# Optimization experiments

Hardware: AMD Instinct MI355X
Metric: run time of the kernel (lower is better)

The kernel has to match this reference:

```python
import jax, jax.numpy as jnp
import numpy as np

D_MODEL = 1024
NUM_HEADS = 16
D_K = D_MODEL // NUM_HEADS


def setup_inputs() -> dict:
    key = jax.random.key(0)
    ks = jax.random.split(key, 11)
    B, S, D = 2, 2048, D_MODEL
    s = 1.0 / np.sqrt(D)  # torch Linear default init scale
    inp = {
        'query': jax.random.normal(ks[0], (B, S, D), jnp.float32),
        'key': jax.random.normal(ks[1], (B, S, D), jnp.float32),
        'value': jax.random.normal(ks[2], (B, S, D), jnp.float32),
        'Wq': jax.random.uniform(ks[3], (D, D), jnp.float32, -s, s),
        'bq': jax.random.uniform(ks[4], (D,), jnp.float32, -s, s),
        'Wk': jax.random.uniform(ks[5], (D, D), jnp.float32, -s, s),
        'bk': jax.random.uniform(ks[6], (D,), jnp.float32, -s, s),
        'Wv': jax.random.uniform(ks[7], (D, D), jnp.float32, -s, s),
        'bv': jax.random.uniform(ks[8], (D,), jnp.float32, -s, s),
        'Wo': jax.random.uniform(ks[9], (D, D), jnp.float32, -s, s),
        'bo': jax.random.uniform(ks[10], (D,), jnp.float32, -s, s),
    }
    return inp


def reference(query, key, value, Wq, bq, Wk, bk, Wv, bv, Wo, bo):
    B, S, D = query.shape
    H, dk = NUM_HEADS, D_K
    # Linear projections (torch Linear: x @ W.T + b), split into heads -> [B,H,S,dk]
    Q = (query @ Wq.T + bq).reshape(B, S, H, dk).transpose(0, 2, 1, 3)
    K = (key @ Wk.T + bk).reshape(B, S, H, dk).transpose(0, 2, 1, 3)
    V = (value @ Wv.T + bv).reshape(B, S, H, dk).transpose(0, 2, 1, 3)
    scale = jnp.sqrt(jnp.asarray(dk, query.dtype))
    scores = jnp.einsum('bhqd,bhkd->bhqk', Q, K) / scale  # [B,H,S,S]
    attn = jax.nn.softmax(scores, axis=-1)
    ctx = jnp.einsum('bhqk,bhkd->bhqd', attn, V)  # [B,H,S,dk]
    ctx = ctx.transpose(0, 2, 1, 3).reshape(B, S, D)
    return ctx @ Wo.T + bo
```

## Files before the change

### kernel.cpp

```cpp
#include <hip/hip_runtime.h>

#define SEQ 2048
#define DM  1024
#define NH  16
#define DK  64
#define BATCH 2
#define MROWS (BATCH * SEQ)
#define PPITCH 72

typedef __attribute__((ext_vector_type(8))) short bf16x8;
typedef __attribute__((ext_vector_type(4))) float f32x4;

__device__ __forceinline__ float bf2f(unsigned short u) {
    union { unsigned int i; float f; } v;
    v.i = ((unsigned int)u) << 16;
    return v.f;
}

__device__ __forceinline__ unsigned short f2bf(float f) {
    union { float f; unsigned int i; } v;
    v.f = f;
    unsigned int r = v.i + 0x7FFFu + ((v.i >> 16) & 1u);
    return (unsigned short)(r >> 16);
}

__device__ __forceinline__ uint4 pack8(float4 x, float4 y) {
    uint4 r;
    r.x = (unsigned)f2bf(x.x) | ((unsigned)f2bf(x.y) << 16);
    r.y = (unsigned)f2bf(x.z) | ((unsigned)f2bf(x.w) << 16);
    r.z = (unsigned)f2bf(y.x) | ((unsigned)f2bf(y.y) << 16);
    r.w = (unsigned)f2bf(y.z) | ((unsigned)f2bf(y.w) << 16);
    return r;
}

__device__ __forceinline__ void gll16(const void* g, void* l) {
    __builtin_amdgcn_global_load_lds(
        (const __attribute__((address_space(1))) unsigned int*)g,
        (__attribute__((address_space(3))) unsigned int*)l, 16, 0, 0);
}

__global__ void detect_dtype(const unsigned short* __restrict__ q,
                             unsigned int* __restrict__ flag) {
    const int lane = threadIdx.x;
    unsigned short u = q[lane * 2];
    int e = (u >> 7) & 0xFF;
    int hit = (e >= 100 && e <= 135) ? 1 : 0;
    unsigned long long m = __ballot(hit);
    if (lane == 0) *flag = (__popcll(m) >= 48) ? 0u : 1u;
}

#define CVT_TOTAL 16781312u
struct CvtArgs {
    const void* src[11];
    unsigned short* dst[11];
};

__global__ __launch_bounds__(256) void convert_all(CvtArgs a,
                                                   const unsigned int* __restrict__ flagp) {
    const unsigned int f = *flagp;
    const size_t e0 = ((size_t)blockIdx.x * 256 + threadIdx.x) * 8;
    if (e0 >= CVT_TOTAL) return;
    const unsigned int cum[12] = {0u, 4194304u, 8388608u, 12582912u, 13631488u,
                                  14680064u, 15728640u, 16777216u, 16778240u,
                                  16779264u, 16780288u, 16781312u};
    int r = 0;
    #pragma unroll
    for (int i = 1; i < 11; ++i) r += (e0 >= cum[i]) ? 1 : 0;
    const size_t local = e0 - cum[r];
    const float sc = (r == 3 || r == 7) ? 0.125f : 1.0f;
    if (f) {
        const float* s = (const float*)a.src[r] + local;
        float4 x = *(const float4*)s;
        float4 y = *(const float4*)(s + 4);
        x.x *= sc; x.y *= sc; x.z *= sc; x.w *= sc;
        y.x *= sc; y.y *= sc; y.z *= sc; y.w *= sc;
        *(uint4*)(a.dst[r] + local) = pack8(x, y);
    } else {
        const unsigned short* s = (const unsigned short*)a.src[r] + local;
        if (sc != 1.0f) {
            unsigned short o[8];
            #pragma unroll
            for (int i = 0; i < 8; ++i) o[i] = f2bf(bf2f(s[i]) * sc);
            *(uint4*)(a.dst[r] + local) = *(const uint4*)o;
        } else {
            *(uint4*)(a.dst[r] + local) = *(const uint4*)s;
        }
    }
}

__device__ __forceinline__ void gemm_core(
    const unsigned short* __restrict__ A, const unsigned short* __restrict__ W,
    const unsigned short* __restrict__ bias, void* __restrict__ C, int cMode)
{
    __shared__ unsigned short Al[64 * 64];
    __shared__ unsigned short Bl[128 * 64];

    const int tid  = threadIdx.x;
    const int w    = tid >> 6;
    const int lane = tid & 63;
    const int lo   = lane & 15;
    const int quad = lane >> 4;
    const int bm   = blockIdx.y * 64;
    const int bn   = blockIdx.x * 128;

    const int r8  = lane >> 3;
    const int csw = ((lane ^ r8) & 7) * 8;
    const unsigned short* gA = A + (size_t)(bm + w * 16 + r8) * DM + csw;
    const unsigned short* gB = W + (size_t)(bn + w * 32 + r8) * DM + csw;
    unsigned short* lA = &Al[(w * 16) * 64];
    unsigned short* lB = &Bl[(w * 32) * 64];

    f32x4 acc[4][2];
    #pragma unroll
    for (int i = 0; i < 4; ++i)
        #pragma unroll
        for (int n = 0; n < 2; ++n) acc[i][n] = (f32x4){0.f, 0.f, 0.f, 0.f};

    const int swz = (lo & 7);

    for (int k0 = 0; k0 < DM; k0 += 64) {
        __syncthreads();
        #pragma unroll
        for (int j = 0; j < 2; ++j)
            gll16(gA + (size_t)j * 8 * DM + k0, lA + j * 8 * 64);
        #pragma unroll
        for (int j = 0; j < 4; ++j)
            gll16(gB + (size_t)j * 8 * DM + k0, lB + j * 8 * 64);
        __syncthreads();

        #pragma unroll
        for (int kc = 0; kc < 2; ++kc) {
            bf16x8 af[4], bfr[2];
            #pragma unroll
            for (int i = 0; i < 4; ++i)
                af[i] = *(const bf16x8*)&Al[(i * 16 + lo) * 64 +
                                            (((kc * 4 + quad) ^ swz) * 8)];
            #pragma unroll
            for (int n = 0; n < 2; ++n)
                bfr[n] = *(const bf16x8*)&Bl[(w * 32 + n * 16 + lo) * 64 +
                                             (((kc * 4 + quad) ^ swz) * 8)];
            #pragma unroll
            for (int i = 0; i < 4; ++i)
                #pragma unroll
                for (int n = 0; n < 2; ++n)
                    acc[i][n] = __builtin_amdgcn_mfma_f32_16x16x32_bf16(af[i], bfr[n], acc[i][n], 0, 0, 0);
        }
    }

    float bj[2];
    #pragma unroll
    for (int n = 0; n < 2; ++n)
        bj[n] = bf2f(bias[bn + w * 32 + n * 16 + lo]);

    if (cMode == 2) {
        #pragma unroll
        for (int i = 0; i < 4; ++i)
            #pragma unroll
            for (int n = 0; n < 2; ++n) {
                const int row0 = bm + i * 16 + quad * 4;
                const int col  = bn + w * 32 + n * 16 + lo;
                ushort4 cv;
                cv.x = f2bf(acc[i][n][0] + bj[n]);
                cv.y = f2bf(acc[i][n][1] + bj[n]);
                cv.z = f2bf(acc[i][n][2] + bj[n]);
                cv.w = f2bf(acc[i][n][3] + bj[n]);
                const size_t off = ((size_t)((row0 >> 11) * 16 + (col >> 6)) * 64
                                    + (col & 63)) * 2048 + (row0 & 2047);
                *(ushort4*)((unsigned short*)C + off) = cv;
            }
    } else {
        #pragma unroll
        for (int i = 0; i < 4; ++i)
            #pragma unroll
            for (int n = 0; n < 2; ++n)
                #pragma unroll
                for (int r = 0; r < 4; ++r) {
                    const int row = bm + i * 16 + quad * 4 + r;
                    const size_t off = (size_t)row * DM + bn + w * 32 + n * 16 + lo;
                    const float vv = acc[i][n][r] + bj[n];
                    if (cMode == 1) ((float*)C)[off] = vv;
                    else            ((unsigned short*)C)[off] = f2bf(vv);
                }
    }
}

__global__ __launch_bounds__(256, 4) void gemm_qkv(
    const unsigned short* __restrict__ qa, const unsigned short* __restrict__ ka,
    const unsigned short* __restrict__ va,
    const unsigned short* __restrict__ wq, const unsigned short* __restrict__ wk,
    const unsigned short* __restrict__ wv,
    const unsigned short* __restrict__ bq, const unsigned short* __restrict__ bk,
    const unsigned short* __restrict__ bv,
    unsigned short* __restrict__ oq, unsigned short* __restrict__ ok,
    unsigned short* __restrict__ ovT)
{
    if (blockIdx.z == 0)      gemm_core(qa, wq, bq, oq, 0);
    else if (blockIdx.z == 1) gemm_core(ka, wk, bk, ok, 0);
    else                      gemm_core(va, wv, bv, ovT, 2);
}

__global__ __launch_bounds__(256, 4) void gemm_out(
    const unsigned short* __restrict__ A, const unsigned short* __restrict__ W,
    const unsigned short* __restrict__ B, void* __restrict__ C,
    const unsigned int* __restrict__ flagp)
{
    gemm_core(A, W, B, C, (int)*flagp);
}

__global__ __launch_bounds__(256) void attn_mfma2(
    const unsigned short* __restrict__ Q,
    const unsigned short* __restrict__ K,
    const unsigned short* __restrict__ VT,
    unsigned short* __restrict__ CTX)
{
    __shared__ unsigned short Kl[64 * 64];
    __shared__ unsigned short Vl[64 * 64];
    __shared__ unsigned short Pl[4][2][16 * PPITCH];

    const int tid  = threadIdx.x;
    const int w    = tid >> 6;
    const int lane = tid & 63;
    const int lo   = lane & 15;
    const int quad = lane >> 4;
    const int bh = blockIdx.y;
    const int b  = bh >> 4;
    const int h  = bh & 15;
    const int q0 = blockIdx.x * 128 + w * 32;

    bf16x8 aq[2][2];
    #pragma unroll
    for (int f = 0; f < 2; ++f)
        #pragma unroll
        for (int c = 0; c < 2; ++c)
            aq[f][c] = *(const bf16x8*)(Q + (size_t)(b * SEQ + q0 + f * 16 + lo) * DM
                                        + h * 64 + c * 32 + quad * 8);

    f32x4 o[2][4];
    #pragma unroll
    for (int f = 0; f < 2; ++f)
        #pragma unroll
        for (int dt = 0; dt < 4; ++dt) o[f][dt] = (f32x4){0.f, 0.f, 0.f, 0.f};
    float lsum[2] = {0.f, 0.f};

    const int r8  = lane >> 3;
    const int csw = ((lane ^ r8) & 7) * 8;
    const int swz = lo & 7;
    const unsigned short* Kg = K + (size_t)b * SEQ * DM + h * 64;
    const unsigned short* Vg = VT + (size_t)bh * 64 * 2048;

    for (int j0 = 0; j0 < SEQ; j0 += 64) {
        __syncthreads();
        #pragma unroll
        for (int j = 0; j < 2; ++j) {
            gll16(Kg + (size_t)(j0 + w * 16 + j * 8 + r8) * DM + csw,
                  &Kl[(w * 16 + j * 8) * 64]);
            gll16(Vg + (size_t)(w * 16 + j * 8 + r8) * 2048 + j0 + csw,
                  &Vl[(w * 16 + j * 8) * 64]);
        }
        __syncthreads();

        f32x4 st[4][2];
        #pragma unroll
        for (int kt = 0; kt < 4; ++kt) {
            bf16x8 ak0 = *(const bf16x8*)&Kl[(kt * 16 + lo) * 64 + ((quad ^ swz) * 8)];
            bf16x8 ak1 = *(const bf16x8*)&Kl[(kt * 16 + lo) * 64 + (((4 + quad) ^ swz) * 8)];
            #pragma unroll
            for (int f = 0; f < 2; ++f) {
                f32x4 c = (f32x4){0.f, 0.f, 0.f, 0.f};
                c = __builtin_amdgcn_mfma_f32_16x16x32_bf16(ak0, aq[f][0], c, 0, 0, 0);
                c = __builtin_amdgcn_mfma_f32_16x16x32_bf16(ak1, aq[f][1], c, 0, 0, 0);
                st[kt][f] = c;
            }
        }

        #pragma unroll
        for (int f = 0; f < 2; ++f)
            #pragma unroll
            for (int kt = 0; kt < 4; ++kt) {
                float p0 = __expf(st[kt][f][0]), p1 = __expf(st[kt][f][1]);
                float p2 = __expf(st[kt][f][2]), p3 = __expf(st[kt][f][3]);
                lsum[f] += (p0 + p1) + (p2 + p3);
                ushort4 pv;
                pv.x = f2bf(p0); pv.y = f2bf(p1); pv.z = f2bf(p2); pv.w = f2bf(p3);
                *(ushort4*)&Pl[w][f][lo * PPITCH + kt * 16 + quad * 4] = pv;
            }
        bf16x8 ap[2][2];
        #pragma unroll
        for (int f = 0; f < 2; ++f)
            #pragma unroll
            for (int c = 0; c < 2; ++c)
                ap[f][c] = *(const bf16x8*)&Pl[w][f][lo * PPITCH + c * 32 + quad * 8];

        #pragma unroll
        for (int dt = 0; dt < 4; ++dt) {
            bf16x8 bv0 = *(const bf16x8*)&Vl[(dt * 16 + lo) * 64 + ((quad ^ swz) * 8)];
            bf16x8 bv1 = *(const bf16x8*)&Vl[(dt * 16 + lo) * 64 + (((4 + quad) ^ swz) * 8)];
            #pragma unroll
            for (int f = 0; f < 2; ++f) {
                o[f][dt] = __builtin_amdgcn_mfma_f32_16x16x32_bf16(ap[f][0], bv0, o[f][dt], 0, 0, 0);
                o[f][dt] = __builtin_amdgcn_mfma_f32_16x16x32_bf16(ap[f][1], bv1, o[f][dt], 0, 0, 0);
            }
        }
    }

    #pragma unroll
    for (int f = 0; f < 2; ++f) {
        lsum[f] += __shfl_xor(lsum[f], 16);
        lsum[f] += __shfl_xor(lsum[f], 32);
    }
    #pragma unroll
    for (int f = 0; f < 2; ++f)
        #pragma unroll
        for (int r = 0; r < 4; ++r) {
            const float lq  = __shfl(lsum[f], quad * 4 + r);
            const float inv = 1.0f / lq;
            const size_t base = (size_t)(b * SEQ + q0 + f * 16 + quad * 4 + r) * DM
                                + h * 64 + lo;
            #pragma unroll
            for (int dt = 0; dt < 4; ++dt)
                CTX[base + dt * 16] = f2bf(o[f][dt][r] * inv);
        }
}

extern "C" void kernel_launch(void* const* d_in, const int* in_sizes, int n_in,
                              void* d_out, int out_size, void* d_ws, size_t ws_size,
                              hipStream_t stream) {
    const size_t E4 = 4194304, E1 = 1048576;
    unsigned short* qb  = (unsigned short*)d_ws;
    unsigned short* kb  = qb  + E4;
    unsigned short* vb  = kb  + E4;
    unsigned short* wqb = vb  + E4;
    unsigned short* wkb = wqb + E1;
    unsigned short* wvb = wkb + E1;
    unsigned short* wob = wvb + E1;
    unsigned short* bqb = wob + E1;
    unsigned short* bkb = bqb + 1024;
    unsigned short* bvb = bkb + 1024;
    unsigned short* bob = bvb + 1024;
    unsigned short* wsQ = bob + 1024;
    unsigned short* wsK = wsQ + E4;
    unsigned short* wsVt = wsK + E4;
    unsigned int*  flag = (unsigned int*)(wsVt + E4);
    unsigned short* wsC = qb;

    detect_dtype<<<1, 64, 0, stream>>>((const unsigned short*)d_in[0], flag);

    CvtArgs ca;
    ca.src[0] = d_in[0];  ca.dst[0] = qb;
    ca.src[1] = d_in[1];  ca.dst[1] = kb;
    ca.src[2] = d_in[2];  ca.dst[2] = vb;
    ca.src[3] = d_in[3];  ca.dst[3] = wqb;
    ca.src[4] = d_in[5];  ca.dst[4] = wkb;
    ca.src[5] = d_in[7];  ca.dst[5] = wvb;
    ca.src[6] = d_in[9];  ca.dst[6] = wob;
    ca.src[7] = d_in[4];  ca.dst[7] = bqb;
    ca.src[8] = d_in[6];  ca.dst[8] = bkb;
    ca.src[9] = d_in[8];  ca.dst[9] = bvb;
    ca.src[10] = d_in[10]; ca.dst[10] = bob;
    convert_all<<<(CVT_TOTAL / 8 + 255) / 256, 256, 0, stream>>>(ca, flag);

    dim3 gq(DM / 128, MROWS / 64, 3);
    gemm_qkv<<<gq, 256, 0, stream>>>(qb, kb, vb, wqb, wkb, wvb,
                                     bqb, bkb, bvb, wsQ, wsK, wsVt);

    dim3 ga(SEQ / 128, BATCH * NH);
    attn_mfma2<<<ga, 256, 0, stream>>>(wsQ, wsK, wsVt, wsC);

    dim3 go(DM / 128, MROWS / 64);
    gemm_out<<<go, 256, 0, stream>>>(wsC, wob, bob, d_out, flag);
}
```

Before: 244.0 us.

## Use exp2 with folded log2e scale, truncating bf16 pack, and MFMA row sums

Folds log2(e)/sqrt(dk) into the Q weight/bias conversion scale so the softmax can use the native exp2 instruction directly. It replaces round-to-nearest bf16 packing of probabilities with a single byte-permute truncation. It computes the softmax denominator by multiplying the bf16 P tile against a ones vector on the matrix cores, which removes the per-element scalar adds and end-of-loop shuffles. The denominator now sums the same rounded bf16 values used in P·V, which keeps normalization consistent, but truncation adds a small bias and each tile costs extra MFMAs.

```diff
diff --git a/kernel.cpp b/kernel.cpp
--- a/kernel.cpp
+++ b/kernel.cpp
@@ -11,6 +11,8 @@
 typedef __attribute__((ext_vector_type(8))) short bf16x8;
 typedef __attribute__((ext_vector_type(4))) float f32x4;
 
+extern "C" __device__ float __ocml_native_exp2_f32(float);
+
 __device__ __forceinline__ float bf2f(unsigned short u) {
     union { unsigned int i; float f; } v;
     v.i = ((unsigned int)u) << 16;
@@ -22,6 +24,11 @@
     v.f = f;
     unsigned int r = v.i + 0x7FFFu + ((v.i >> 16) & 1u);
     return (unsigned short)(r >> 16);
+}
+
+__device__ __forceinline__ unsigned int pk_trunc(float a, float b) {
+    return __builtin_amdgcn_perm(__float_as_uint(b), __float_as_uint(a),
+                                 0x07060302u);
 }
 
 __device__ __forceinline__ uint4 pack8(float4 x, float4 y) {
@@ -49,6 +56,7 @@
     if (lane == 0) *flag = (__popcll(m) >= 48) ? 0u : 1u;
 }
 
+#define QSCALE 0.1803368801111204f
 #define CVT_TOTAL 16781312u
 struct CvtArgs {
     const void* src[11];
@@ -67,7 +75,7 @@
     #pragma unroll
     for (int i = 1; i < 11; ++i) r += (e0 >= cum[i]) ? 1 : 0;
     const size_t local = e0 - cum[r];
-    const float sc = (r == 3 || r == 7) ? 0.125f : 1.0f;
+    const float sc = (r == 3 || r == 7) ? QSCALE : 1.0f;
     if (f) {
         const float* s = (const float*)a.src[r] + local;
         float4 x = *(const float4*)s;
@@ -240,7 +248,12 @@
     for (int f = 0; f < 2; ++f)
         #pragma unroll
         for (int dt = 0; dt < 4; ++dt) o[f][dt] = (f32x4){0.f, 0.f, 0.f, 0.f};
-    float lsum[2] = {0.f, 0.f};
+    f32x4 lacc[2];
+    lacc[0] = (f32x4){0.f, 0.f, 0.f, 0.f};
+    lacc[1] = (f32x4){0.f, 0.f, 0.f, 0.f};
+
+    const short one_s = (short)0x3F80;
+    const bf16x8 ones = {one_s, one_s, one_s, one_s, one_s, one_s, one_s, one_s};
 
     const int r8  = lane >> 3;
     const int csw = ((lane ^ r8) & 7) * 8;
@@ -277,12 +290,14 @@
         for (int f = 0; f < 2; ++f)
             #pragma unroll
             for (int kt = 0; kt < 4; ++kt) {
-                float p0 = __expf(st[kt][f][0]), p1 = __expf(st[kt][f][1]);
-                float p2 = __expf(st[kt][f][2]), p3 = __expf(st[kt][f][3]);
-                lsum[f] += (p0 + p1) + (p2 + p3);
-                ushort4 pv;
-                pv.x = f2bf(p0); pv.y = f2bf(p1); pv.z = f2bf(p2); pv.w = f2bf(p3);
-                *(ushort4*)&Pl[w][f][lo * PPITCH + kt * 16 + quad * 4] = pv;
+                float p0 = __ocml_native_exp2_f32(st[kt][f][0]);
+                float p1 = __ocml_native_exp2_f32(st[kt][f][1]);
+                float p2 = __ocml_native_exp2_f32(st[kt][f][2]);
+                float p3 = __ocml_native_exp2_f32(st[kt][f][3]);
+                uint2 pv;
+                pv.x = pk_trunc(p0, p1);
+                pv.y = pk_trunc(p2, p3);
+                *(uint2*)&Pl[w][f][lo * PPITCH + kt * 16 + quad * 4] = pv;
             }
         bf16x8 ap[2][2];
         #pragma unroll
@@ -290,6 +305,12 @@
             #pragma unroll
             for (int c = 0; c < 2; ++c)
                 ap[f][c] = *(const bf16x8*)&Pl[w][f][lo * PPITCH + c * 32 + quad * 8];
+
+        #pragma unroll
+        for (int f = 0; f < 2; ++f) {
+            lacc[f] = __builtin_amdgcn_mfma_f32_16x16x32_bf16(ap[f][0], ones, lacc[f], 0, 0, 0);
+            lacc[f] = __builtin_amdgcn_mfma_f32_16x16x32_bf16(ap[f][1], ones, lacc[f], 0, 0, 0);
+        }
 
         #pragma unroll
         for (int dt = 0; dt < 4; ++dt) {
@@ -304,16 +325,10 @@
     }
 
     #pragma unroll
-    for (int f = 0; f < 2; ++f) {
-        lsum[f] += __shfl_xor(lsum[f], 16);
-        lsum[f] += __shfl_xor(lsum[f], 32);
-    }
-    #pragma unroll
     for (int f = 0; f < 2; ++f)
         #pragma unroll
         for (int r = 0; r < 4; ++r) {
-            const float lq  = __shfl(lsum[f], quad * 4 + r);
-            const float inv = 1.0f / lq;
+            const float inv = 1.0f / lacc[f][r];
             const size_t base = (size_t)(b * SEQ + q0 + f * 16 + quad * 4 + r) * DM
                                 + h * 64 + lo;
             #pragma unroll
```

Measured after the change: 239.0 us. 1.02x faster.
